# Performance work log

Measured on AMD Instinct MI355X. Metric: run time of the kernel, lower is better.

The kernel has to match this reference:

```python
import jax, jax.numpy as jnp
import numpy as np

D_MODEL = 512
N_HEADS = 8
D_K = D_MODEL // N_HEADS


def setup_inputs() -> dict:
    key = jax.random.key(0)
    ks = jax.random.split(key, 12)
    B, L = 2, 512
    s = 1.0 / np.sqrt(D_MODEL)
    sk = 1.0 / np.sqrt(D_K)
    return {
        "query": jax.random.normal(ks[0], (B, L, D_MODEL), jnp.float32),
        "key": jax.random.normal(ks[1], (B, L, D_MODEL), jnp.float32),
        "value": jax.random.normal(ks[2], (B, L, D_MODEL), jnp.float32),
        "Wq": jax.random.normal(ks[3], (D_MODEL, D_MODEL), jnp.float32) * s,
        "bq": jnp.zeros((D_MODEL,), jnp.float32),
        "Wk": jax.random.normal(ks[4], (D_MODEL, D_MODEL), jnp.float32) * s,
        "bk": jnp.zeros((D_MODEL,), jnp.float32),
        "Wv": jax.random.normal(ks[5], (D_MODEL, D_MODEL), jnp.float32) * s,
        "bv": jnp.zeros((D_MODEL,), jnp.float32),
        "Wo": jax.random.normal(ks[6], (D_MODEL, D_MODEL), jnp.float32) * s,
        "bo": jnp.zeros((D_MODEL,), jnp.float32),
        "Aq": jax.random.normal(ks[7], (D_K, D_K), jnp.float32) * sk,  # inner W_q (no bias)
        "Ak": jax.random.normal(ks[8], (D_K, D_K), jnp.float32) * sk,  # inner W_k (no bias)
        "av": jax.random.normal(ks[9], (D_K,), jnp.float32) * sk,      # inner v (d_k -> 1)
    }


def _split_heads(x):
    B, L, _ = x.shape
    return x.reshape(B, L, N_HEADS, D_K).transpose(0, 2, 1, 3)  # [B,H,L,dk]


def reference(query, key, value, Wq, bq, Wk, bk, Wv, bv, Wo, bo, Aq, Ak, av):
    # outer projections (torch Linear: x @ W.T + b)
    Q = _split_heads(query @ Wq.T + bq)   # [B,H,Lq,dk]
    K = _split_heads(key @ Wk.T + bk)     # [B,H,Lk,dk]
    V = _split_heads(value @ Wv.T + bv)   # [B,H,Lk,dk]
    # inner additive attention: e_ij = v^T tanh(Aq q_i + Ak k_j)
    qp = Q @ Aq.T                          # [B,H,Lq,dk]
    kp = K @ Ak.T                          # [B,H,Lk,dk]
    energy = jnp.tanh(qp[:, :, :, None, :] + kp[:, :, None, :, :])  # [B,H,Lq,Lk,dk]
    scores = jnp.einsum('bhqkd,d->bhqk', energy, av)
    attn = jax.nn.softmax(scores, axis=-1)  # dropout disabled (eval)
    out = jnp.einsum('bhqk,bhkd->bhqd', attn, V)  # [B,H,Lq,dk]
    B, _, Lq, _ = out.shape
    out = out.transpose(0, 2, 1, 3).reshape(B, Lq, D_MODEL)
    return out @ Wo.T + bo
```

## Files before the change

kernel.cpp:

```cpp
#include <hip/hip_runtime.h>

#define LOG2E 1.4426950408889634f

typedef __bf16 bf16x8 __attribute__((ext_vector_type(8)));
typedef float f32x4 __attribute__((ext_vector_type(4)));
typedef float f32x2 __attribute__((ext_vector_type(2)));

__device__ __forceinline__ unsigned short bfb(__bf16 b){
  union { __bf16 b; unsigned short u; } z; z.b = b; return z.u;
}
__device__ __forceinline__ void split8(const float* p, bf16x8& hi, bf16x8& lo){
  #pragma unroll
  for (int j = 0; j < 8; j++){
    float f = p[j];
    __bf16 h = (__bf16)f;
    hi[j] = h;
    lo[j] = (__bf16)(f - (float)h);
  }
}


__global__ __launch_bounds__(256) void prep_all(
    const float* __restrict__ Wq, const float* __restrict__ Aq,
    const float* __restrict__ Wk, const float* __restrict__ Ak,
    const float* __restrict__ bq, const float* __restrict__ bk,
    const float* __restrict__ av,
    const float* __restrict__ Wv, const float* __restrict__ Wo,
    unsigned short* __restrict__ W2qp, unsigned short* __restrict__ W2kp,
    unsigned short* __restrict__ Wvp,  unsigned short* __restrict__ Wop,
    float* __restrict__ b2q, float* __restrict__ b2k, float* __restrict__ av2g){
  if (blockIdx.x >= 256){
    if (blockIdx.x == 512){
      if (blockIdx.y == 0){
        #pragma unroll
        for (int rep = 0; rep < 2; rep++){
          int n = rep * 256 + threadIdx.x;
          int h = n >> 6, e = n & 63;
          float aq = 0.f, ak = 0.f;
          for (int c = 0; c < 64; c++){
            aq += Aq[e*64 + c] * bq[h*64 + c];
            ak += Ak[e*64 + c] * bk[h*64 + c];
          }
          b2q[n] = aq * (2.f * LOG2E);
          b2k[n] = ak * (2.f * LOG2E);
        }
      } else {
        if (threadIdx.x < 64) av2g[threadIdx.x] = -2.f * LOG2E * av[threadIdx.x];
      }
      return;
    }
    const float* src = blockIdx.y ? Wo : Wv;
    unsigned short* dst = blockIdx.y ? Wop : Wvp;
    int base = ((blockIdx.x - 256) * 256 + threadIdx.x) * 4;
    int n = base >> 9, k0 = base & 511;
    float4 v = *(const float4*)(src + base);
    ushort4 h, l;
    float f; __bf16 hb;
    f = v.x; hb = (__bf16)f; h.x = bfb(hb); l.x = bfb((__bf16)(f - (float)hb));
    f = v.y; hb = (__bf16)f; h.y = bfb(hb); l.y = bfb((__bf16)(f - (float)hb));
    f = v.z; hb = (__bf16)f; h.z = bfb(hb); l.z = bfb((__bf16)(f - (float)hb));
    f = v.w; hb = (__bf16)f; h.w = bfb(hb); l.w = bfb((__bf16)(f - (float)hb));
    int nt = n >> 4, ln = n & 15;
    int ks = k0 >> 5, q = (k0 & 31) >> 3, j0 = k0 & 7;
    size_t off = (size_t)((nt*16 + ks) * 2) * 512 + (q*16 + ln) * 8 + j0;
    *(ushort4*)(dst + off)       = h;
    *(ushort4*)(dst + off + 512) = l;
    return;
  }
  const float* W  = blockIdx.y ? Wk : Wq;
  const float* Am = blockIdx.y ? Ak : Aq;
  unsigned short* dst = blockIdx.y ? W2kp : W2qp;
  int idx = blockIdx.x * 256 + threadIdx.x;
  int n = idx >> 7;
  int k0 = (idx & 127) * 4;
  int h = n >> 6, e = n & 63;
  float4 acc = {0.f, 0.f, 0.f, 0.f};
  #pragma unroll 8
  for (int c = 0; c < 64; c++){
    float am = Am[e*64 + c];
    float4 wv = *(const float4*)(W + (size_t)(h*64 + c)*512 + k0);
    acc.x += am * wv.x;
    acc.y += am * wv.y;
    acc.z += am * wv.z;
    acc.w += am * wv.w;
  }
  int nt = n >> 4, ln = n & 15;
  int ks = k0 >> 5, q = (k0 & 31) >> 3, j0 = k0 & 7;
  size_t off = (size_t)((nt*16 + ks) * 2) * 512 + (q*16 + ln) * 8 + j0;
  ushort4 hh, ll;
  float f; __bf16 hb;
  f = acc.x * (2.f * LOG2E); hb = (__bf16)f; hh.x = bfb(hb); ll.x = bfb((__bf16)(f - (float)hb));
  f = acc.y * (2.f * LOG2E); hb = (__bf16)f; hh.y = bfb(hb); ll.y = bfb((__bf16)(f - (float)hb));
  f = acc.z * (2.f * LOG2E); hb = (__bf16)f; hh.z = bfb(hb); ll.z = bfb((__bf16)(f - (float)hb));
  f = acc.w * (2.f * LOG2E); hb = (__bf16)f; hh.w = bfb(hb); ll.w = bfb((__bf16)(f - (float)hb));
  *(ushort4*)(dst + off)       = hh;
  *(ushort4*)(dst + off + 512) = ll;
}

struct GemmBatch {
  const float* Af;
  const unsigned short* Bp;
  const float* bias;
  float* Cf;
  int transposed;
  int expout;
};
struct GemmArgs { GemmBatch g[3]; };

__global__ __launch_bounds__(256) void gemm_nk(GemmArgs ga){
  GemmBatch gb = ga.g[blockIdx.z];
  __shared__ float As[64 * 68];
  const int tid = threadIdx.x, lane = tid & 63, w = tid >> 6;
  const int l15 = lane & 15, quad = lane >> 4;
  const int m0  = blockIdx.x * 64;
  const int nt0 = blockIdx.y * 4;
  f32x4 ac0 = {0.f,0.f,0.f,0.f}, ac1 = ac0, ac2 = ac0, ac3 = ac0;

  const int sr = tid >> 2;
  const int sc = (tid & 3) * 16;
  const float* srcA = gb.Af + (size_t)(m0 + sr) * 512 + sc;
  float* dstA = &As[sr * 68 + sc];

  for (int kc = 0; kc < 8; kc++){
    __syncthreads();
    #pragma unroll
    for (int i = 0; i < 4; i++)
      *(f32x4*)(dstA + i*4) = *(const f32x4*)(srcA + kc*64 + i*4);
    __syncthreads();
    #pragma unroll
    for (int s = 0; s < 2; s++){
      int ks = kc * 2 + s;
      bf16x8 ah, al;
      split8(&As[(w*16 + l15) * 68 + s*32 + quad*8], ah, al);
      #pragma unroll
      for (int t = 0; t < 4; t++){
        const unsigned short* bp = gb.Bp + (size_t)(((nt0 + t)*16 + ks) * 2) * 512 + lane*8;
        bf16x8 bh = *(const bf16x8*)bp;
        bf16x8 bl = *(const bf16x8*)(bp + 512);
        f32x4& ac = (t==0)?ac0:(t==1)?ac1:(t==2)?ac2:ac3;
        ac = __builtin_amdgcn_mfma_f32_16x16x32_bf16(ah, bh, ac, 0, 0, 0);
        ac = __builtin_amdgcn_mfma_f32_16x16x32_bf16(al, bh, ac, 0, 0, 0);
        ac = __builtin_amdgcn_mfma_f32_16x16x32_bf16(ah, bl, ac, 0, 0, 0);
      }
    }
  }

  const int mrow = m0 + w * 16 + quad * 4;
  #pragma unroll
  for (int t = 0; t < 4; t++){
    f32x4 v = (t==0)?ac0:(t==1)?ac1:(t==2)?ac2:ac3;
    int n = nt0 * 16 + t * 16 + l15;
    float bs = gb.bias[n];
    #pragma unroll
    for (int r = 0; r < 4; r++){
      float val = v[r] + bs;
      if (gb.expout) val = __builtin_amdgcn_exp2f(val);
      int m2 = mrow + r;
      if (gb.transposed){
        gb.Cf[(size_t)(((m2 >> 9) * 8 + (n >> 6)) * 64 + (n & 63)) * 512 + (m2 & 511)] = val;
      } else {
        gb.Cf[(size_t)m2 * 512 + n] = val;
      }
    }
  }
}

__global__ __launch_bounds__(1024, 8) void attn_kernel(
    const float* __restrict__ eqT, const float* __restrict__ ekp,
    const float* __restrict__ Vv, const float* __restrict__ av2g,
    float* __restrict__ Oh){
  __shared__ float bufA[64 * 130];
  __shared__ float bufB[64 * 130];
  __shared__ unsigned short pcb[2 * 16 * 136];
  __shared__ float dn[16];
  float* cmb = bufA;

  const int tid = threadIdx.x, lane = tid & 63, w = tid >> 6;
  const int l15 = lane & 15, quad = lane >> 4;
  const int bh = blockIdx.y;
  const int i0 = blockIdx.x * 16;
  const size_t kbase = (size_t)(bh >> 3) * 512 * 512 + (size_t)(bh & 7) * 64;
  const int r0 = __builtin_amdgcn_readfirstlane(w);
  const size_t qbase = (size_t)bh * 64 * 512 + i0 + r0;
  const int ntile = w & 3, kq = w >> 2;

  float den = 0.f;
  f32x4 Cacc = {0.f, 0.f, 0.f, 0.f};

  {
    #pragma unroll
    for (int m = 0; m < 4; m++){
      int i = w + 16 * m;
      float a = ekp[kbase + (size_t)(2*i    ) * 512 + lane];
      float b = ekp[kbase + (size_t)(2*i + 1) * 512 + lane];
      *(float2*)&bufA[lane * 130 + 2*i] = make_float2(a, b);
    }
  }
  __syncthreads();

  for (int c = 0; c < 4; c++){
    float va[4], vb[4];
    #pragma unroll
    for (int m = 0; m < 4; m++){
      int i = w + 16 * m;
      va[m] = Vv[kbase + (size_t)(c*128 + 2*i    ) * 512 + lane];
      vb[m] = Vv[kbase + (size_t)(c*128 + 2*i + 1) * 512 + lane];
    }
    f32x2 sacc = {0.f, 0.f};
    #pragma unroll 8
    for (int d = 0; d < 64; d += 2){
      float eq0 = eqT[qbase + (size_t)d * 512];
      float eq1 = eqT[qbase + (size_t)(d+1) * 512];
      float a0 = av2g[d];
      float a1 = av2g[d+1];
      f32x2 ek0 = *(const f32x2*)&bufA[d * 130 + 2 * lane];
      f32x2 ek1 = *(const f32x2*)&bufA[(d+1) * 130 + 2 * lane];
      f32x2 A = __builtin_elementwise_fma((f32x2){eq0, eq0}, ek0, (f32x2){1.f, 1.f});
      f32x2 B = __builtin_elementwise_fma((f32x2){eq1, eq1}, ek1, (f32x2){1.f, 1.f});
      f32x2 t = (f32x2){a0, a0} * B;
      t = __builtin_elementwise_fma((f32x2){a1, a1}, A, t);
      f32x2 dpr = A * B;
      f32x2 r;
      r.x = __builtin_amdgcn_rcpf(dpr.x);
      r.y = __builtin_amdgcn_rcpf(dpr.y);
      sacc = __builtin_elementwise_fma(t, r, sacc);
    }
    float e0 = __builtin_amdgcn_exp2f(sacc.x);
    float e1 = __builtin_amdgcn_exp2f(sacc.y);
    den += e0 + e1;
    {
      __bf16 h0 = (__bf16)e0, h1 = (__bf16)e1;
      ushort2 hi = { bfb(h0), bfb(h1) };
      ushort2 lo = { bfb((__bf16)(e0 - (float)h0)), bfb((__bf16)(e1 - (float)h1)) };
      *(ushort2*)&pcb[(0*16 + r0) * 136 + 2*lane] = hi;
      *(ushort2*)&pcb[(1*16 + r0) * 136 + 2*lane] = lo;
    }
    #pragma unroll
    for (int m = 0; m < 4; m++){
      int i = w + 16 * m;
      *(float2*)&bufB[lane * 130 + 2*i] = make_float2(va[m], vb[m]);
    }
    __syncthreads();

    float ka[4], kb[4];
    if (c < 3){
      #pragma unroll
      for (int m = 0; m < 4; m++){
        int i = w + 16 * m;
        ka[m] = ekp[kbase + (size_t)((c+1)*128 + 2*i    ) * 512 + lane];
        kb[m] = ekp[kbase + (size_t)((c+1)*128 + 2*i + 1) * 512 + lane];
      }
    }
    {
      int k0 = kq * 32 + quad * 8;
      bf16x8 ph = *(const bf16x8*)&pcb[(0*16 + l15) * 136 + k0];
      bf16x8 pl = *(const bf16x8*)&pcb[(1*16 + l15) * 136 + k0];
      const float* vp = &bufB[(ntile*16 + l15) * 130 + k0];
      bf16x8 vh, vl;
      #pragma unroll
      for (int j = 0; j < 8; j++){
        float f = vp[j];
        __bf16 h = (__bf16)f;
        vh[j] = h; vl[j] = (__bf16)(f - (float)h);
      }
      Cacc = __builtin_amdgcn_mfma_f32_16x16x32_bf16(ph, vh, Cacc, 0, 0, 0);
      Cacc = __builtin_amdgcn_mfma_f32_16x16x32_bf16(pl, vh, Cacc, 0, 0, 0);
      Cacc = __builtin_amdgcn_mfma_f32_16x16x32_bf16(ph, vl, Cacc, 0, 0, 0);
    }
    if (c < 3){
      #pragma unroll
      for (int m = 0; m < 4; m++){
        int i = w + 16 * m;
        *(float2*)&bufA[lane * 130 + 2*i] = make_float2(ka[m], kb[m]);
      }
    }
    __syncthreads();
  }

  #pragma unroll
  for (int off = 1; off < 64; off <<= 1)
    den += __shfl_xor(den, off, 64);
  if (lane == 0) dn[r0] = den;
  if (kq > 0){
    #pragma unroll
    for (int r = 0; r < 4; r++) cmb[(w - 4) * 256 + lane * 4 + r] = Cacc[r];
  }
  __syncthreads();
  if (kq == 0){
    #pragma unroll
    for (int r = 0; r < 4; r++){
      float cv = Cacc[r];
      #pragma unroll
      for (int j = 0; j < 3; j++) cv += cmb[(j*4 + ntile) * 256 + lane * 4 + r];
      int row = quad * 4 + r;
      int d = ntile * 16 + l15;
      Oh[kbase + (size_t)(i0 + row) * 512 + d] = cv / dn[row];
    }
  }
}

extern "C" void kernel_launch(void* const* d_in, const int* in_sizes, int n_in,
                              void* d_out, int out_size, void* d_ws, size_t ws_size,
                              hipStream_t stream){
  const float* q_in = (const float*)d_in[0];
  const float* k_in = (const float*)d_in[1];
  const float* v_in = (const float*)d_in[2];
  const float* Wq_  = (const float*)d_in[3];
  const float* bq_  = (const float*)d_in[4];
  const float* Wk_  = (const float*)d_in[5];
  const float* bk_  = (const float*)d_in[6];
  const float* Wv_  = (const float*)d_in[7];
  const float* bv_  = (const float*)d_in[8];
  const float* Wo_  = (const float*)d_in[9];
  const float* bo_  = (const float*)d_in[10];
  const float* Aq_  = (const float*)d_in[11];
  const float* Ak_  = (const float*)d_in[12];
  const float* av_  = (const float*)d_in[13];

  char* ws = (char*)d_ws;
  unsigned short* W2qp = (unsigned short*)(ws + 0);
  unsigned short* W2kp = (unsigned short*)(ws + 1048576);
  float* Oh = (float*)(ws + 0);
  unsigned short* Wvp = (unsigned short*)(ws + 2097152);
  unsigned short* Wop = (unsigned short*)(ws + 3145728);
  float* b2q  = (float*)(ws + 4194304);
  float* b2k  = (float*)(ws + 4196352);
  float* av2g = (float*)(ws + 4198400);
  float* eqT  = (float*)(ws + 4198656);
  float* ekp  = (float*)(ws + 6295808);
  float* Vw   = (float*)(ws + 8392960);

  prep_all<<<dim3(513, 2, 1), 256, 0, stream>>>(Wq_, Aq_, Wk_, Ak_, bq_, bk_, av_,
                                                Wv_, Wo_,
                                                W2qp, W2kp, Wvp, Wop,
                                                b2q, b2k, av2g);

  GemmArgs ga;
  ga.g[0] = { q_in, W2qp, b2q, eqT, 1, 1 };
  ga.g[1] = { k_in, W2kp, b2k, ekp, 0, 1 };
  ga.g[2] = { v_in, Wvp,  bv_, Vw,  0, 0 };
  gemm_nk<<<dim3(16, 8, 3), 256, 0, stream>>>(ga);

  attn_kernel<<<dim3(32, 16, 1), 1024, 0, stream>>>(eqT, ekp, Vw, av2g, Oh);

  GemmArgs go;
  go.g[0] = { Oh, Wop, bo_, (float*)d_out, 0, 0 };
  go.g[1] = go.g[0];
  go.g[2] = go.g[0];
  gemm_nk<<<dim3(16, 8, 1), 256, 0, stream>>>(go);
}
```

Measured before the change: 163.4 us.

## Stage query features in LDS with head-major layout and prefetch next key tile earlier

The query-side GEMM now writes its exponentiated output as [b,h,i,d] instead of transposed [b,h,d,i]. The attention kernel loads each block's 16 query rows and the av2 vector into shared memory once, then reads them as float4 vectors from LDS instead of issuing scalar global loads inside the inner reduction loop. The prefetch of the next key tile is moved ahead of the score computation to overlap its global latency with the math. The cost is extra shared memory and registers, which may reduce occupancy, and the query GEMM's stores become less coalesced.

```diff
diff --git a/kernel.cpp b/kernel.cpp
--- a/kernel.cpp
+++ b/kernel.cpp
@@ -157,7 +157,7 @@
       if (gb.expout) val = __builtin_amdgcn_exp2f(val);
       int m2 = mrow + r;
       if (gb.transposed){
-        gb.Cf[(size_t)(((m2 >> 9) * 8 + (n >> 6)) * 64 + (n & 63)) * 512 + (m2 & 511)] = val;
+        gb.Cf[(size_t)(((m2 >> 9) * 8 + (n >> 6)) * 512 + (m2 & 511)) * 64 + (n & 63)] = val;
       } else {
         gb.Cf[(size_t)m2 * 512 + n] = val;
       }
@@ -166,13 +166,15 @@
 }
 
 __global__ __launch_bounds__(1024, 8) void attn_kernel(
-    const float* __restrict__ eqT, const float* __restrict__ ekp,
+    const float* __restrict__ eqQ, const float* __restrict__ ekp,
     const float* __restrict__ Vv, const float* __restrict__ av2g,
     float* __restrict__ Oh){
   __shared__ float bufA[64 * 130];
   __shared__ float bufB[64 * 130];
   __shared__ unsigned short pcb[2 * 16 * 136];
   __shared__ float dn[16];
+  __shared__ float eqs[16 * 64];
+  __shared__ float avs[64];
   float* cmb = bufA;
 
   const int tid = threadIdx.x, lane = tid & 63, w = tid >> 6;
@@ -181,13 +183,14 @@
   const int i0 = blockIdx.x * 16;
   const size_t kbase = (size_t)(bh >> 3) * 512 * 512 + (size_t)(bh & 7) * 64;
   const int r0 = __builtin_amdgcn_readfirstlane(w);
-  const size_t qbase = (size_t)bh * 64 * 512 + i0 + r0;
   const int ntile = w & 3, kq = w >> 2;
 
   float den = 0.f;
   f32x4 Cacc = {0.f, 0.f, 0.f, 0.f};
 
   {
+    eqs[w * 64 + lane] = eqQ[((size_t)bh * 512 + i0 + w) * 64 + lane];
+    if (w == 0) avs[lane] = av2g[lane];
     #pragma unroll
     for (int m = 0; m < 4; m++){
       int i = w + 16 * m;
@@ -199,31 +202,46 @@
   __syncthreads();
 
   for (int c = 0; c < 4; c++){
-    float va[4], vb[4];
+    float va[4], vb[4], ka[4], kb[4];
     #pragma unroll
     for (int m = 0; m < 4; m++){
       int i = w + 16 * m;
       va[m] = Vv[kbase + (size_t)(c*128 + 2*i    ) * 512 + lane];
       vb[m] = Vv[kbase + (size_t)(c*128 + 2*i + 1) * 512 + lane];
     }
+    if (c < 3){
+      #pragma unroll
+      for (int m = 0; m < 4; m++){
+        int i = w + 16 * m;
+        ka[m] = ekp[kbase + (size_t)((c+1)*128 + 2*i    ) * 512 + lane];
+        kb[m] = ekp[kbase + (size_t)((c+1)*128 + 2*i + 1) * 512 + lane];
+      }
+    }
     f32x2 sacc = {0.f, 0.f};
-    #pragma unroll 8
-    for (int d = 0; d < 64; d += 2){
-      float eq0 = eqT[qbase + (size_t)d * 512];
-      float eq1 = eqT[qbase + (size_t)(d+1) * 512];
-      float a0 = av2g[d];
-      float a1 = av2g[d+1];
-      f32x2 ek0 = *(const f32x2*)&bufA[d * 130 + 2 * lane];
+    #pragma unroll 4
+    for (int d = 0; d < 64; d += 4){
+      f32x4 eq4 = *(const f32x4*)&eqs[r0 * 64 + d];
+      f32x4 a4  = *(const f32x4*)&avs[d];
+      f32x2 ek0 = *(const f32x2*)&bufA[(d  ) * 130 + 2 * lane];
       f32x2 ek1 = *(const f32x2*)&bufA[(d+1) * 130 + 2 * lane];
-      f32x2 A = __builtin_elementwise_fma((f32x2){eq0, eq0}, ek0, (f32x2){1.f, 1.f});
-      f32x2 B = __builtin_elementwise_fma((f32x2){eq1, eq1}, ek1, (f32x2){1.f, 1.f});
-      f32x2 t = (f32x2){a0, a0} * B;
-      t = __builtin_elementwise_fma((f32x2){a1, a1}, A, t);
+      f32x2 ek2 = *(const f32x2*)&bufA[(d+2) * 130 + 2 * lane];
+      f32x2 ek3 = *(const f32x2*)&bufA[(d+3) * 130 + 2 * lane];
+      f32x2 A = __builtin_elementwise_fma((f32x2){eq4[0], eq4[0]}, ek0, (f32x2){1.f, 1.f});
+      f32x2 B = __builtin_elementwise_fma((f32x2){eq4[1], eq4[1]}, ek1, (f32x2){1.f, 1.f});
+      f32x2 t = __builtin_elementwise_fma((f32x2){a4[1], a4[1]}, A, (f32x2){a4[0], a4[0]} * B);
       f32x2 dpr = A * B;
       f32x2 r;
       r.x = __builtin_amdgcn_rcpf(dpr.x);
       r.y = __builtin_amdgcn_rcpf(dpr.y);
       sacc = __builtin_elementwise_fma(t, r, sacc);
+      f32x2 C = __builtin_elementwise_fma((f32x2){eq4[2], eq4[2]}, ek2, (f32x2){1.f, 1.f});
+      f32x2 D = __builtin_elementwise_fma((f32x2){eq4[3], eq4[3]}, ek3, (f32x2){1.f, 1.f});
+      f32x2 t2 = __builtin_elementwise_fma((f32x2){a4[3], a4[3]}, C, (f32x2){a4[2], a4[2]} * D);
+      f32x2 dpr2 = C * D;
+      f32x2 r2;
+      r2.x = __builtin_amdgcn_rcpf(dpr2.x);
+      r2.y = __builtin_amdgcn_rcpf(dpr2.y);
+      sacc = __builtin_elementwise_fma(t2, r2, sacc);
     }
     float e0 = __builtin_amdgcn_exp2f(sacc.x);
     float e1 = __builtin_amdgcn_exp2f(sacc.y);
@@ -242,15 +260,6 @@
     }
     __syncthreads();
 
-    float ka[4], kb[4];
-    if (c < 3){
-      #pragma unroll
-      for (int m = 0; m < 4; m++){
-        int i = w + 16 * m;
-        ka[m] = ekp[kbase + (size_t)((c+1)*128 + 2*i    ) * 512 + lane];
-        kb[m] = ekp[kbase + (size_t)((c+1)*128 + 2*i + 1) * 512 + lane];
-      }
-    }
     {
       int k0 = kq * 32 + quad * 8;
       bf16x8 ph = *(const bf16x8*)&pcb[(0*16 + l15) * 136 + k0];
@@ -326,7 +335,7 @@
   float* b2q  = (float*)(ws + 4194304);
   float* b2k  = (float*)(ws + 4196352);
   float* av2g = (float*)(ws + 4198400);
-  float* eqT  = (float*)(ws + 4198656);
+  float* eqQ  = (float*)(ws + 4198656);
   float* ekp  = (float*)(ws + 6295808);
   float* Vw   = (float*)(ws + 8392960);
 
@@ -336,12 +345,12 @@
                                                 b2q, b2k, av2g);
 
   GemmArgs ga;
-  ga.g[0] = { q_in, W2qp, b2q, eqT, 1, 1 };
+  ga.g[0] = { q_in, W2qp, b2q, eqQ, 1, 1 };
   ga.g[1] = { k_in, W2kp, b2k, ekp, 0, 1 };
   ga.g[2] = { v_in, Wvp,  bv_, Vw,  0, 0 };
   gemm_nk<<<dim3(16, 8, 3), 256, 0, stream>>>(ga);
 
-  attn_kernel<<<dim3(32, 16, 1), 1024, 0, stream>>>(eqT, ekp, Vw, av2g, Oh);
+  attn_kernel<<<dim3(32, 16, 1), 1024, 0, stream>>>(eqQ, ekp, Vw, av2g, Oh);
 
   GemmArgs go;
   go.g[0] = { Oh, Wop, bo_, (float*)d_out, 0, 0 };
```

Measured after the change: 161.3 us. Within noise of the previous version (-1.2%).
